# Kernel tuning notes

Measured on AMD Instinct MI355X. Metric: run time of the kernel, lower is better.

## Reference

```python
import jax, jax.numpy as jnp
import numpy as np

B, Hdim, Wdim, C, HEADS, WS = 16, 112, 112, 128, 4, 7
VD = C
MLP_H = int(4.0 * VD)
EPS = 1e-5


def _layernorm(x, g, b):
    mu = jnp.mean(x, axis=-1, keepdims=True)
    var = jnp.mean(jnp.square(x - mu), axis=-1, keepdims=True)
    return (x - mu) * jax.lax.rsqrt(var + EPS) * g + b


def _rel_pos_index(ws):
    # static numpy computation, identical to the torch buffer
    coords = np.stack(np.meshgrid(np.arange(ws), np.arange(ws), indexing='ij'))  # (2, ws, ws)
    cf = coords.reshape(2, -1)                       # (2, N)
    rel = cf[:, :, None] - cf[:, None, :]            # (2, N, N)
    rel = rel.transpose(1, 2, 0).copy()              # (N, N, 2)
    rel[:, :, 0] += ws - 1
    rel[:, :, 1] += ws - 1
    rel[:, :, 0] *= 2 * ws - 1
    return jnp.asarray(rel.sum(-1))                  # (N, N) int


def setup_inputs() -> dict:
    key = jax.random.key(0)
    ks = jax.random.split(key, 10)
    nrm = lambda k, s: jax.random.normal(k, s, jnp.float32) * 0.02
    return {
        'x': jax.random.normal(ks[0], (B, Hdim * Wdim, C), jnp.float32),
        'v': jax.random.normal(ks[1], (B, Hdim * Wdim, C), jnp.float32),
        'norm1_g': jnp.ones((C,), jnp.float32), 'norm1_b': jnp.zeros((C,), jnp.float32),
        'normv_g': jnp.ones((C,), jnp.float32), 'normv_b': jnp.zeros((C,), jnp.float32),
        'q_w': nrm(ks[2], (C, C)), 'q_b': jnp.zeros((C,), jnp.float32),
        'kv_w': nrm(ks[3], (2 * C, C)), 'kv_b': jnp.zeros((2 * C,), jnp.float32),
        'rpb_table': nrm(ks[4], ((2 * WS - 1) ** 2, HEADS)),
        'proj_w': nrm(ks[5], (VD, VD)), 'proj_b': jnp.zeros((VD,), jnp.float32),
        'norm2_g': jnp.ones((VD,), jnp.float32), 'norm2_b': jnp.zeros((VD,), jnp.float32),
        'fc1_w': nrm(ks[6], (MLP_H, VD)), 'fc1_b': jnp.zeros((MLP_H,), jnp.float32),
        'fc2_w': nrm(ks[7], (VD, MLP_H)), 'fc2_b': jnp.zeros((VD,), jnp.float32),
        'H': Hdim, 'W': Wdim,
    }


def reference(x, v, norm1_g, norm1_b, normv_g, normv_b, q_w, q_b, kv_w, kv_b,
              rpb_table, proj_w, proj_b, norm2_g, norm2_b, fc1_w, fc1_b,
              fc2_w, fc2_b, H, W):
    Bsz, L, Cd = x.shape
    ws = WS
    heads = HEADS
    hd = Cd // heads
    scale = hd ** (-0.5)

    xs = _layernorm(x, norm1_g, norm1_b).reshape(Bsz, H, W, Cd)
    vs = _layernorm(v, normv_g, normv_b).reshape(Bsz, H, W, Cd)

    pad_b = (ws - H % ws) % ws
    pad_r = (ws - W % ws) % ws
    if pad_b or pad_r:
        xs = jnp.pad(xs, ((0, 0), (0, pad_b), (0, pad_r), (0, 0)))
        vs = jnp.pad(vs, ((0, 0), (0, pad_b), (0, pad_r), (0, 0)))
    Hp, Wp = H + pad_b, W + pad_r

    def part(t):  # window partition -> (nW*B, ws*ws, C)
        return t.reshape(Bsz, Hp // ws, ws, Wp // ws, ws, t.shape[-1]) \
                .transpose(0, 1, 3, 2, 4, 5).reshape(-1, ws * ws, t.shape[-1])

    xw = part(xs)
    vw = part(vs)
    N = ws * ws

    q = (xw @ q_w.T + q_b).reshape(-1, N, heads, hd).transpose(0, 2, 1, 3)   # (B_, h, N, d)
    kv = (vw @ kv_w.T + kv_b).reshape(-1, N, 2, heads, hd).transpose(2, 0, 3, 1, 4)
    k, vv = kv[0], kv[1]

    attn = jnp.einsum('bhnd,bhmd->bhnm', q * scale, k)
    rpi = _rel_pos_index(ws)
    bias = rpb_table[rpi.reshape(-1)].reshape(N, N, heads).transpose(2, 0, 1)  # (h, N, N)
    attn = jax.nn.softmax(attn + bias[None], axis=-1)

    out = jnp.einsum('bhnm,bhmd->bhnd', attn, vv).transpose(0, 2, 1, 3).reshape(-1, N, Cd)
    out = out @ proj_w.T + proj_b

    # window reverse
    out = out.reshape(Bsz, Hp // ws, Wp // ws, ws, ws, VD) \
             .transpose(0, 1, 3, 2, 4, 5).reshape(Bsz, Hp, Wp, VD)
    out = out[:, :H, :W, :].reshape(Bsz, H * W, VD)

    xo = out + x  # residual with pre-norm shortcut
    h = _layernorm(xo, norm2_g, norm2_b)
    h = jax.nn.gelu(h @ fc1_w.T + fc1_b, approximate=False)
    h = h @ fc2_w.T + fc2_b
    return xo + h
```

## Files before the change

### kernel.cpp

```cpp
#include <hip/hip_runtime.h>
#include <hip/hip_bf16.h>
#include <math.h>

typedef __hip_bfloat16 bf16;
typedef __hip_bfloat162 bf162;
typedef __attribute__((ext_vector_type(8))) short bf16x8;
typedef __attribute__((ext_vector_type(4))) short short4v;
typedef __attribute__((ext_vector_type(4))) float f32x4;

__device__ __forceinline__ float b2f(bf16 x){ return __bfloat162float(x); }
__device__ __forceinline__ bf16  f2b(float x){ return __float2bfloat16(x); }
__device__ __forceinline__ short f2bs(float x){ bf16 h = __float2bfloat16(x); return *(short*)&h; }

constexpr int kH = 112, kW = 112, kC = 128, kHeads = 4, kWS = 7;
constexpr int kN = 49, kHD = 32, kL = kH * kW;
constexpr int kWinElems = kN * kC;
constexpr int kMLP = 512;
constexpr float kEps = 1e-5f;
constexpr float kScale = 0.17677669529663687f;
constexpr int kAP = 136;
constexpr int kHP = 520;
constexpr int kXP = 132;

__global__ __launch_bounds__(256) void k_cvt(
    const float* __restrict__ qw, const float* __restrict__ kvw,
    const float* __restrict__ pw, const float* __restrict__ w1,
    const float* __restrict__ w2, short* __restrict__ dst)
{
    const int i = blockIdx.x * 256 + threadIdx.x;
    float val;
    if (i < 16384)       val = qw[i];
    else if (i < 49152)  val = kvw[i - 16384];
    else if (i < 65536)  val = pw[i - 49152];
    else if (i < 131072) val = w1[i - 65536];
    else                 val = w2[i - 131072];
    dst[i] = f2bs(val);
}

__global__ __launch_bounds__(256) void k_ln_qkv_mfma(
    const float* __restrict__ x, const float* __restrict__ v,
    const float* __restrict__ n1g, const float* __restrict__ n1b,
    const float* __restrict__ nvg, const float* __restrict__ nvb,
    const short* __restrict__ qwb, const float* __restrict__ qb,
    const short* __restrict__ kvwb, const float* __restrict__ kvb,
    bf16* __restrict__ qo, bf16* __restrict__ ko, bf16* __restrict__ vo)
{
    __shared__ short Xs[32 * kAP], Vs[32 * kAP];
    const int tid = threadIdx.x, wave = tid >> 6, lane = tid & 63;
    const int quad = lane >> 4, l16 = lane & 15;
    const int row0 = blockIdx.x * 32;
    const int c0 = lane * 2;

    for (int n = wave; n < 32; n += 4) {
        const size_t r = (size_t)(row0 + n) * kC;
        const float2 xv = *(const float2*)(x + r + c0);
        const float2 vv = *(const float2*)(v + r + c0);
        float sx = xv.x + xv.y, qx = xv.x * xv.x + xv.y * xv.y;
        float sv = vv.x + vv.y, qv = vv.x * vv.x + vv.y * vv.y;
        #pragma unroll
        for (int off = 32; off > 0; off >>= 1) {
            sx += __shfl_xor(sx, off); qx += __shfl_xor(qx, off);
            sv += __shfl_xor(sv, off); qv += __shfl_xor(qv, off);
        }
        const float mux = sx * (1.f / kC);
        const float ivx = rsqrtf(qx * (1.f / kC) - mux * mux + kEps);
        const float muv = sv * (1.f / kC);
        const float ivv = rsqrtf(qv * (1.f / kC) - muv * muv + kEps);
        Xs[n * kAP + c0]     = f2bs((xv.x - mux) * ivx * n1g[c0] + n1b[c0]);
        Xs[n * kAP + c0 + 1] = f2bs((xv.y - mux) * ivx * n1g[c0 + 1] + n1b[c0 + 1]);
        Vs[n * kAP + c0]     = f2bs((vv.x - muv) * ivv * nvg[c0] + nvb[c0]);
        Vs[n * kAP + c0 + 1] = f2bs((vv.y - muv) * ivv * nvg[c0 + 1] + nvb[c0 + 1]);
    }
    __syncthreads();

    int woff[2];
    #pragma unroll
    for (int mt = 0; mt < 2; mt++) {
        const int gr = row0 + mt * 16 + l16;
        const int b = gr / kL, l = gr - b * kL;
        const int h = l / kW, w_ = l - h * kW;
        woff[mt] = ((b << 8) + (h / 7) * 16 + (w_ / 7)) * kWinElems
                 + ((h % 7) * 7 + (w_ % 7)) * kC;
    }

    bf16x8 xf[2][4], vf[2][4];
    #pragma unroll
    for (int mt = 0; mt < 2; mt++)
        #pragma unroll
        for (int ks = 0; ks < 4; ks++) {
            xf[mt][ks] = *(const bf16x8*)&Xs[(mt * 16 + l16) * kAP + ks * 32 + quad * 8];
            vf[mt][ks] = *(const bf16x8*)&Vs[(mt * 16 + l16) * kAP + ks * 32 + quad * 8];
        }

    #pragma unroll
    for (int j = 0; j < 6; j++) {
        const int nt = wave * 6 + j;
        const bool isq = (nt < 8);
        const short* wmat = isq ? qwb : kvwb;
        const int wr0 = (isq ? nt : nt - 8) * 16;
        const float* bias = isq ? qb : kvb;
        const int bidx = wr0 + quad * 4;
        f32x4 a0 = { bias[bidx], bias[bidx + 1], bias[bidx + 2], bias[bidx + 3] };
        f32x4 a1 = a0;
        if (isq) {
            #pragma unroll
            for (int ks = 0; ks < 4; ks++) {
                const bf16x8 af = *(const bf16x8*)(wmat + (size_t)(wr0 + l16) * kC + ks * 32 + quad * 8);
                a0 = __builtin_amdgcn_mfma_f32_16x16x32_bf16(af, xf[0][ks], a0, 0, 0, 0);
                a1 = __builtin_amdgcn_mfma_f32_16x16x32_bf16(af, xf[1][ks], a1, 0, 0, 0);
            }
        } else {
            #pragma unroll
            for (int ks = 0; ks < 4; ks++) {
                const bf16x8 af = *(const bf16x8*)(wmat + (size_t)(wr0 + l16) * kC + ks * 32 + quad * 8);
                a0 = __builtin_amdgcn_mfma_f32_16x16x32_bf16(af, vf[0][ks], a0, 0, 0, 0);
                a1 = __builtin_amdgcn_mfma_f32_16x16x32_bf16(af, vf[1][ks], a1, 0, 0, 0);
            }
        }
        bf16* dst = isq ? qo : (nt < 16 ? ko : vo);
        const int cb = (isq ? nt : (nt < 16 ? nt - 8 : nt - 16)) * 16 + quad * 4;
        short4v p0, p1;
        #pragma unroll
        for (int i = 0; i < 4; i++) { p0[i] = f2bs(a0[i]); p1[i] = f2bs(a1[i]); }
        *(short4v*)((short*)dst + (size_t)woff[0] + cb) = p0;
        *(short4v*)((short*)dst + (size_t)woff[1] + cb) = p1;
    }
}

__global__ __launch_bounds__(256, 3) void k_attn_mfma(
    bf16* __restrict__ qbuf, const bf16* __restrict__ kbuf,
    const bf16* __restrict__ vbuf, const float* __restrict__ rpb)
{
    __shared__ short Pl[kHeads][64 * 64];
    __shared__ short Vt[kHeads][32 * 64];
    __shared__ float rpl[kHeads][169];
    const int tid = threadIdx.x, wave = tid >> 6, lane = tid & 63;
    const int quad = lane >> 4, l16 = lane & 15;
    const int head = wave;
    const size_t wbase = (size_t)blockIdx.x * kWinElems;

    for (int i = lane; i < 169; i += 64) rpl[head][i] = rpb[i * kHeads + head];

    bf16x8 qf[4], kf[4];
    const bf16* qp = qbuf + wbase + head * kHD + quad * 8;
    const bf16* kp = kbuf + wbase + head * kHD + quad * 8;
    #pragma unroll
    for (int t = 0; t < 4; t++) {
        qf[t] = *(const bf16x8*)(qp + (size_t)(t * 16 + l16) * kC);
        kf[t] = *(const bf16x8*)(kp + (size_t)(t * 16 + l16) * kC);
    }

    #pragma unroll
    for (int h = 0; h < 4; h++) {
        for (int i = tid; i < 1024; i += 256) {
            const int m = i >> 4, d2 = (i & 15) << 1;
            int val = 0;
            if (m < 49) val = *(const int*)(vbuf + wbase + (size_t)m * kC + h * kHD + d2);
            Vt[h][d2 * 64 + (m ^ ((d2 & 7) << 3))]         = (short)(val & 0xffff);
            Vt[h][(d2 + 1) * 64 + (m ^ (((d2 + 1) & 7) << 3))] = (short)(val >> 16);
        }
    }

    f32x4 S[4][4];
    #pragma unroll
    for (int nt = 0; nt < 4; nt++)
        #pragma unroll
        for (int mt = 0; mt < 4; mt++)
            S[nt][mt] = __builtin_amdgcn_mfma_f32_16x16x32_bf16(
                qf[nt], kf[mt], (f32x4){0.f, 0.f, 0.f, 0.f}, 0, 0, 0);

    __syncthreads();

    int an[4][4];
    #pragma unroll
    for (int nt = 0; nt < 4; nt++)
        #pragma unroll
        for (int i = 0; i < 4; i++) {
            const int n = nt * 16 + quad * 4 + i;
            an[nt][i] = 13 * (n / 7) + (n % 7) + 84;
        }
    int bm[4]; bool mok[4];
    #pragma unroll
    for (int mt = 0; mt < 4; mt++) {
        const int m = mt * 16 + l16;
        bm[mt] = 13 * (m / 7) + (m % 7);
        mok[mt] = (m < 49);
    }

    const float* rp = rpl[head];
    #pragma unroll
    for (int nt = 0; nt < 4; nt++)
        #pragma unroll
        for (int i = 0; i < 4; i++) {
            float sv[4];
            #pragma unroll
            for (int mt = 0; mt < 4; mt++) {
                int idx = an[nt][i] - bm[mt];
                idx = ((unsigned)idx > 168u) ? 0 : idx;
                sv[mt] = mok[mt] ? (S[nt][mt][i] * kScale + rp[idx]) : -1e30f;
            }
            float mx = fmaxf(fmaxf(sv[0], sv[1]), fmaxf(sv[2], sv[3]));
            #pragma unroll
            for (int off = 1; off < 16; off <<= 1) mx = fmaxf(mx, __shfl_xor(mx, off));
            float e[4];
            float sum = 0.f;
            #pragma unroll
            for (int mt = 0; mt < 4; mt++) { e[mt] = __expf(sv[mt] - mx); sum += e[mt]; }
            #pragma unroll
            for (int off = 1; off < 16; off <<= 1) sum += __shfl_xor(sum, off);
            const float inv = 1.f / sum;
            const int prow = nt * 16 + quad * 4 + i;
            short* pr = &Pl[head][prow * 64];
            const int sw = (prow & 7) << 3;
            #pragma unroll
            for (int mt = 0; mt < 4; mt++)
                pr[(mt * 16 + l16) ^ sw] = f2bs(e[mt] * inv);
        }

    bf16x8 va[2][2], pb2[4][2];
    #pragma unroll
    for (int dt = 0; dt < 2; dt++)
        #pragma unroll
        for (int ks = 0; ks < 2; ks++) {
            const int r = dt * 16 + l16;
            va[dt][ks] = *(const bf16x8*)&Vt[head][r * 64 + ((ks * 32 + quad * 8) ^ ((r & 7) << 3))];
        }
    #pragma unroll
    for (int nt = 0; nt < 4; nt++)
        #pragma unroll
        for (int ks = 0; ks < 2; ks++) {
            const int r = nt * 16 + l16;
            pb2[nt][ks] = *(const bf16x8*)&Pl[head][r * 64 + ((ks * 32 + quad * 8) ^ ((r & 7) << 3))];
        }
    f32x4 o[2][4];
    #pragma unroll
    for (int dt = 0; dt < 2; dt++)
        #pragma unroll
        for (int nt = 0; nt < 4; nt++) {
            f32x4 a = __builtin_amdgcn_mfma_f32_16x16x32_bf16(
                va[dt][0], pb2[nt][0], (f32x4){0.f, 0.f, 0.f, 0.f}, 0, 0, 0);
            o[dt][nt] = __builtin_amdgcn_mfma_f32_16x16x32_bf16(
                va[dt][1], pb2[nt][1], a, 0, 0, 0);
        }

    #pragma unroll
    for (int nt = 0; nt < 4; nt++) {
        const int n = nt * 16 + l16;
        if (n < 49) {
            bf16* dst = qbuf + wbase + (size_t)n * kC + head * kHD + quad * 4;
            #pragma unroll
            for (int dt = 0; dt < 2; dt++) {
                short4v p;
                #pragma unroll
                for (int i = 0; i < 4; i++) p[i] = f2bs(o[dt][nt][i]);
                *(short4v*)(dst + dt * 16) = p;
            }
        }
    }
}

constexpr int kMT = 32;

__global__ __launch_bounds__(256, 3) void k_proj_mlp(
    const bf16* __restrict__ ao, const short* __restrict__ pwb,
    const float* __restrict__ pb, const float* __restrict__ x,
    float* __restrict__ out,
    const float* __restrict__ g2, const float* __restrict__ b2v,
    const short* __restrict__ w1b, const float* __restrict__ bb1,
    const short* __restrict__ w2b, const float* __restrict__ bb2)
{
    __shared__ float Xo[kMT * kXP];
    __shared__ short U[kMT * kHP];
    short* const As  = U;
    short* const A_s = U;
    short* const H_s = U;
    const int tid = threadIdx.x, wave = tid >> 6, lane = tid & 63;
    const int quad = lane >> 4, l16 = lane & 15;
    const size_t row0 = (size_t)blockIdx.x * kMT;
    const int c0 = lane * 2;

    for (int n = wave; n < 32; n += 4) {
        const int gr = (int)row0 + n;
        const int b = gr / kL, l = gr - b * kL;
        const int h = l / kW, w_ = l - h * kW;
        const size_t off = (size_t)(((b << 8) + (h / 7) * 16 + (w_ / 7))) * kWinElems
                         + ((h % 7) * 7 + (w_ % 7)) * kC;
        *(int*)&As[n * kAP + c0] = *(const int*)((const short*)ao + off + c0);
    }
    __syncthreads();

    bf16x8 bfrag[2][4];
    #pragma unroll
    for (int mt = 0; mt < 2; mt++)
        #pragma unroll
        for (int ks = 0; ks < 4; ks++)
            bfrag[mt][ks] = *(const bf16x8*)&As[(mt * 16 + l16) * kAP + ks * 32 + quad * 8];

    float4 res[2][2];
    #pragma unroll
    for (int j = 0; j < 2; j++)
        #pragma unroll
        for (int mt = 0; mt < 2; mt++)
            res[j][mt] = *(const float4*)(x + (row0 + mt * 16 + l16) * kC
                                            + (wave * 2 + j) * 16 + quad * 4);

    #pragma unroll
    for (int j = 0; j < 2; j++) {
        const int nt = wave * 2 + j;
        const int cb = nt * 16 + quad * 4;
        f32x4 a0 = { pb[cb], pb[cb + 1], pb[cb + 2], pb[cb + 3] };
        f32x4 a1 = a0;
        #pragma unroll
        for (int ks = 0; ks < 4; ks++) {
            const bf16x8 af = *(const bf16x8*)(pwb + (size_t)(nt * 16 + l16) * kC + ks * 32 + quad * 8);
            a0 = __builtin_amdgcn_mfma_f32_16x16x32_bf16(af, bfrag[0][ks], a0, 0, 0, 0);
            a1 = __builtin_amdgcn_mfma_f32_16x16x32_bf16(af, bfrag[1][ks], a1, 0, 0, 0);
        }
        #pragma unroll
        for (int mt = 0; mt < 2; mt++) {
            const f32x4 a = mt ? a1 : a0;
            float4 r = res[j][mt];
            r.x += a[0]; r.y += a[1]; r.z += a[2]; r.w += a[3];
            *(float4*)&Xo[(mt * 16 + l16) * kXP + cb] = r;
        }
    }
    __syncthreads();

    const float gg0 = g2[c0], gg1 = g2[c0 + 1];
    const float bv0 = b2v[c0], bv1 = b2v[c0 + 1];
    float2 xv[8];
    #pragma unroll
    for (int it = 0; it < 8; it++)
        xv[it] = *(const float2*)&Xo[(wave + it * 4) * kXP + c0];
    float s[8], q[8];
    #pragma unroll
    for (int it = 0; it < 8; it++) {
        s[it] = xv[it].x + xv[it].y;
        q[it] = xv[it].x * xv[it].x + xv[it].y * xv[it].y;
    }
    #pragma unroll
    for (int off = 32; off > 0; off >>= 1) {
        #pragma unroll
        for (int it = 0; it < 8; it++) {
            s[it] += __shfl_xor(s[it], off);
            q[it] += __shfl_xor(q[it], off);
        }
    }
    #pragma unroll
    for (int it = 0; it < 8; it++) {
        const int n = wave + it * 4;
        const float mu = s[it] * (1.f / kC);
        const float iv = rsqrtf(q[it] * (1.f / kC) - mu * mu + kEps);
        const short h0 = f2bs((xv[it].x - mu) * iv * gg0 + bv0);
        const short h1 = f2bs((xv[it].y - mu) * iv * gg1 + bv1);
        *(int*)&A_s[n * kAP + c0] =
            ((int)(unsigned short)h1 << 16) | (int)(unsigned short)h0;
    }
    __syncthreads();

    bf16x8 bfrag2[2][4];
    #pragma unroll
    for (int mt = 0; mt < 2; mt++)
        #pragma unroll
        for (int ks = 0; ks < 4; ks++)
            bfrag2[mt][ks] = *(const bf16x8*)&A_s[(mt * 16 + l16) * kAP + ks * 32 + quad * 8];
    __syncthreads();

    const short* wbase = w1b + (size_t)(wave * 128 + l16) * kC + quad * 8;
    auto loadw1 = [&](bf16x8* dst, int t) {
        #pragma unroll
        for (int ks = 0; ks < 4; ks++)
            dst[ks] = *(const bf16x8*)(wbase + (size_t)t * (16 * kC) + ks * 32);
    };
    auto mfma8 = [&](f32x4* a, const bf16x8* w) {
        #pragma unroll
        for (int ks = 0; ks < 4; ks++) {
            a[0] = __builtin_amdgcn_mfma_f32_16x16x32_bf16(w[ks], bfrag2[0][ks], a[0], 0, 0, 0);
            a[1] = __builtin_amdgcn_mfma_f32_16x16x32_bf16(w[ks], bfrag2[1][ks], a[1], 0, 0, 0);
        }
    };
    #pragma unroll
    for (int g = 0; g < 2; g++) {
        f32x4 acc[4][2];
        #pragma unroll
        for (int t = 0; t < 4; t++) {
            const float4 bi = *(const float4*)(bb1 + (wave * 8 + g * 4 + t) * 16 + quad * 4);
            acc[t][0] = (f32x4){ bi.x, bi.y, bi.z, bi.w };
            acc[t][1] = acc[t][0];
        }
        bf16x8 wA[4], wB[4];
        loadw1(wA, g * 4 + 0);
        loadw1(wB, g * 4 + 1);
        mfma8(acc[0], wA);
        loadw1(wA, g * 4 + 2);
        mfma8(acc[1], wB);
        loadw1(wB, g * 4 + 3);
        mfma8(acc[2], wA);
        mfma8(acc[3], wB);
        #pragma unroll
        for (int t = 0; t < 4; t++) {
            const int nb = (wave * 8 + g * 4 + t) * 16 + quad * 4;
            #pragma unroll
            for (int mt = 0; mt < 2; mt++) {
                short4v p;
                #pragma unroll
                for (int i = 0; i < 4; i++) {
                    const float a = acc[t][mt][i];
                    p[i] = f2bs(0.5f * a * (1.f + erff(a * 0.70710678118f)));
                }
                *(short4v*)&H_s[(mt * 16 + l16) * kHP + nb] = p;
            }
        }
    }
    __syncthreads();

    const int ct0 = wave * 2;
    f32x4 acc2[2][2];
    #pragma unroll
    for (int t = 0; t < 2; t++) {
        const float4 bi = *(const float4*)(bb2 + (ct0 + t) * 16 + quad * 4);
        acc2[t][0] = (f32x4){ bi.x, bi.y, bi.z, bi.w };
        acc2[t][1] = acc2[t][0];
    }
    const short* w2base = w2b + (size_t)(ct0 * 16 + l16) * kMLP + quad * 8;
    const short* hbase0 = &H_s[l16 * kHP + quad * 8];
    const short* hbase1 = &H_s[(16 + l16) * kHP + quad * 8];
    auto loadh = [&](bf16x8* h, bf16x8* w, int kk) {
        h[0] = *(const bf16x8*)(hbase0 + kk * 32);
        h[1] = *(const bf16x8*)(hbase1 + kk * 32);
        w[0] = *(const bf16x8*)(w2base + kk * 32);
        w[1] = *(const bf16x8*)(w2base + (size_t)16 * kMLP + kk * 32);
    };
    auto mfma4 = [&](const bf16x8* h, const bf16x8* w) {
        acc2[0][0] = __builtin_amdgcn_mfma_f32_16x16x32_bf16(w[0], h[0], acc2[0][0], 0, 0, 0);
        acc2[0][1] = __builtin_amdgcn_mfma_f32_16x16x32_bf16(w[0], h[1], acc2[0][1], 0, 0, 0);
        acc2[1][0] = __builtin_amdgcn_mfma_f32_16x16x32_bf16(w[1], h[0], acc2[1][0], 0, 0, 0);
        acc2[1][1] = __builtin_amdgcn_mfma_f32_16x16x32_bf16(w[1], h[1], acc2[1][1], 0, 0, 0);
    };
    bf16x8 hA[2], wwA[2], hB[2], wwB[2];
    loadh(hA, wwA, 0);
    #pragma unroll
    for (int kk = 0; kk < 16; kk += 2) {
        loadh(hB, wwB, kk + 1);
        mfma4(hA, wwA);
        if (kk + 2 < 16) loadh(hA, wwA, kk + 2);
        mfma4(hB, wwB);
    }

    #pragma unroll
    for (int t = 0; t < 2; t++) {
        const int cbv = (ct0 + t) * 16 + quad * 4;
        #pragma unroll
        for (int mt = 0; mt < 2; mt++) {
            const size_t m = row0 + mt * 16 + l16;
            const float4 xo = *(const float4*)&Xo[(mt * 16 + l16) * kXP + cbv];
            float4 r;
            r.x = xo.x + acc2[t][mt][0]; r.y = xo.y + acc2[t][mt][1];
            r.z = xo.z + acc2[t][mt][2]; r.w = xo.w + acc2[t][mt][3];
            *(float4*)(out + m * kC + cbv) = r;
        }
    }
}

extern "C" void kernel_launch(void* const* d_in, const int* in_sizes, int n_in,
                              void* d_out, int out_size, void* d_ws, size_t ws_size,
                              hipStream_t stream) {
    (void)in_sizes; (void)n_in; (void)out_size; (void)ws_size;
    const float* x      = (const float*)d_in[0];
    const float* v      = (const float*)d_in[1];
    const float* n1g    = (const float*)d_in[2];
    const float* n1b    = (const float*)d_in[3];
    const float* nvg    = (const float*)d_in[4];
    const float* nvb    = (const float*)d_in[5];
    const float* q_w    = (const float*)d_in[6];
    const float* q_b    = (const float*)d_in[7];
    const float* kv_w   = (const float*)d_in[8];
    const float* kv_b   = (const float*)d_in[9];
    const float* rpb    = (const float*)d_in[10];
    const float* proj_w = (const float*)d_in[11];
    const float* proj_b = (const float*)d_in[12];
    const float* n2g    = (const float*)d_in[13];
    const float* n2b    = (const float*)d_in[14];
    const float* fc1_w  = (const float*)d_in[15];
    const float* fc1_b  = (const float*)d_in[16];
    const float* fc2_w  = (const float*)d_in[17];
    const float* fc2_b  = (const float*)d_in[18];

    const size_t winTot = (size_t)4096 * kWinElems;
    bf16* qbuf = (bf16*)d_ws;
    bf16* kbuf = qbuf + winTot;
    bf16* vbuf = kbuf + winTot;
    short* wcvt = (short*)(vbuf + winTot);
    short* qwb  = wcvt;
    short* kvwb = qwb + 16384;
    short* pwb  = kvwb + 32768;
    short* w1b  = pwb + 16384;
    short* w2b  = w1b + 65536;
    float* outb = (float*)d_out;

    k_cvt<<<768, 256, 0, stream>>>(q_w, kv_w, proj_w, fc1_w, fc2_w, wcvt);
    k_ln_qkv_mfma<<<6272, 256, 0, stream>>>(x, v, n1g, n1b, nvg, nvb,
                                            qwb, q_b, kvwb, kv_b, qbuf, kbuf, vbuf);
    k_attn_mfma<<<4096, 256, 0, stream>>>(qbuf, kbuf, vbuf, rpb);
    k_proj_mlp<<<6272, 256, 0, stream>>>(qbuf, pwb, proj_b, x, outb,
                                         n2g, n2b, w1b, fc1_b, w2b, fc2_b);
}
```

Baseline: 726.4 us.

## Keep residual in registers, swizzle LDS, and raise proj/MLP occupancy

Reworks k_proj_mlp so the attention output is loaded directly from global memory into MFMA fragments instead of staged through LDS, and the post-projection residual stays in registers rather than in a float LDS buffer. LayerNorm statistics are reduced with shuffles plus a small LDS scratch area. Padded LDS strides are replaced by an XOR swizzle, which shrinks LDS so launch bounds can ask for 4 blocks per CU. One barrier is removed. The cost is more live registers per thread, which may cause spills at the higher occupancy target, and uncoalesced direct global fragment loads.

New measurement: 733.0 us. Within noise of the previous version (+0.9%).

```diff
diff --git a/kernel.cpp b/kernel.cpp
--- a/kernel.cpp
+++ b/kernel.cpp
@@ -19,8 +19,6 @@
 constexpr float kEps = 1e-5f;
 constexpr float kScale = 0.17677669529663687f;
 constexpr int kAP = 136;
-constexpr int kHP = 520;
-constexpr int kXP = 132;
 
 __global__ __launch_bounds__(256) void k_cvt(
     const float* __restrict__ qw, const float* __restrict__ kvw,
@@ -260,8 +258,10 @@
 }
 
 constexpr int kMT = 32;
-
-__global__ __launch_bounds__(256, 3) void k_proj_mlp(
+constexpr int kAPs = 128;
+constexpr int kHPs = 512;
+
+__global__ __launch_bounds__(256, 4) void k_proj_mlp(
     const bf16* __restrict__ ao, const short* __restrict__ pwb,
     const float* __restrict__ pb, const float* __restrict__ x,
     float* __restrict__ out,
@@ -269,32 +269,32 @@
     const short* __restrict__ w1b, const float* __restrict__ bb1,
     const short* __restrict__ w2b, const float* __restrict__ bb2)
 {
-    __shared__ float Xo[kMT * kXP];
-    __shared__ short U[kMT * kHP];
-    short* const As  = U;
-    short* const A_s = U;
-    short* const H_s = U;
+    __shared__ short LDSu[kMT * kAPs + kMT * kHPs];
+    short* const A_s = LDSu;
+    short* const H_s = LDSu + kMT * kAPs;
+    float* const lnscr = (float*)H_s;
+
     const int tid = threadIdx.x, wave = tid >> 6, lane = tid & 63;
     const int quad = lane >> 4, l16 = lane & 15;
     const size_t row0 = (size_t)blockIdx.x * kMT;
-    const int c0 = lane * 2;
-
-    for (int n = wave; n < 32; n += 4) {
-        const int gr = (int)row0 + n;
+    const int xorm = (l16 & 7) << 3;
+
+    int woff[2];
+    #pragma unroll
+    for (int mt = 0; mt < 2; mt++) {
+        const int gr = (int)row0 + mt * 16 + l16;
         const int b = gr / kL, l = gr - b * kL;
         const int h = l / kW, w_ = l - h * kW;
-        const size_t off = (size_t)(((b << 8) + (h / 7) * 16 + (w_ / 7))) * kWinElems
-                         + ((h % 7) * 7 + (w_ % 7)) * kC;
-        *(int*)&As[n * kAP + c0] = *(const int*)((const short*)ao + off + c0);
-    }
-    __syncthreads();
-
+        woff[mt] = ((b << 8) + (h / 7) * 16 + (w_ / 7)) * kWinElems
+                 + ((h % 7) * 7 + (w_ % 7)) * kC;
+    }
     bf16x8 bfrag[2][4];
     #pragma unroll
     for (int mt = 0; mt < 2; mt++)
         #pragma unroll
         for (int ks = 0; ks < 4; ks++)
-            bfrag[mt][ks] = *(const bf16x8*)&As[(mt * 16 + l16) * kAP + ks * 32 + quad * 8];
+            bfrag[mt][ks] = *(const bf16x8*)((const short*)ao
+                                + (size_t)woff[mt] + ks * 32 + quad * 8);
 
     float4 res[2][2];
     #pragma unroll
@@ -303,12 +303,21 @@
         for (int mt = 0; mt < 2; mt++)
             res[j][mt] = *(const float4*)(x + (row0 + mt * 16 + l16) * kC
                                             + (wave * 2 + j) * 16 + quad * 4);
-
+    float4 gv[2], bvv[2];
+    #pragma unroll
+    for (int j = 0; j < 2; j++) {
+        const int cb = (wave * 2 + j) * 16 + quad * 4;
+        gv[j]  = *(const float4*)(g2 + cb);
+        bvv[j] = *(const float4*)(b2v + cb);
+    }
+
+    f32x4 xo[2][2];
     #pragma unroll
     for (int j = 0; j < 2; j++) {
         const int nt = wave * 2 + j;
         const int cb = nt * 16 + quad * 4;
-        f32x4 a0 = { pb[cb], pb[cb + 1], pb[cb + 2], pb[cb + 3] };
+        const float4 pbv = *(const float4*)(pb + cb);
+        f32x4 a0 = { pbv.x, pbv.y, pbv.z, pbv.w };
         f32x4 a1 = a0;
         #pragma unroll
         for (int ks = 0; ks < 4; ks++) {
@@ -317,44 +326,62 @@
             a1 = __builtin_amdgcn_mfma_f32_16x16x32_bf16(af, bfrag[1][ks], a1, 0, 0, 0);
         }
         #pragma unroll
+        for (int i = 0; i < 4; i++) {
+            xo[j][0][i] = a0[i] + ((const float*)&res[j][0])[i];
+            xo[j][1][i] = a1[i] + ((const float*)&res[j][1])[i];
+        }
+    }
+
+    float sp[2], qp[2];
+    #pragma unroll
+    for (int mt = 0; mt < 2; mt++) {
+        float s = 0.f, q = 0.f;
+        #pragma unroll
+        for (int j = 0; j < 2; j++)
+            #pragma unroll
+            for (int i = 0; i < 4; i++) {
+                const float v = xo[j][mt][i];
+                s += v; q += v * v;
+            }
+        s += __shfl_xor(s, 16); q += __shfl_xor(q, 16);
+        s += __shfl_xor(s, 32); q += __shfl_xor(q, 32);
+        sp[mt] = s; qp[mt] = q;
+    }
+    if (quad == 0) {
+        #pragma unroll
         for (int mt = 0; mt < 2; mt++) {
-            const f32x4 a = mt ? a1 : a0;
-            float4 r = res[j][mt];
-            r.x += a[0]; r.y += a[1]; r.z += a[2]; r.w += a[3];
-            *(float4*)&Xo[(mt * 16 + l16) * kXP + cb] = r;
+            float2 pr; pr.x = sp[mt]; pr.y = qp[mt];
+            *(float2*)&lnscr[(mt * 16 + l16) * 8 + wave * 2] = pr;
         }
     }
     __syncthreads();
 
-    const float gg0 = g2[c0], gg1 = g2[c0 + 1];
-    const float bv0 = b2v[c0], bv1 = b2v[c0 + 1];
-    float2 xv[8];
-    #pragma unroll
-    for (int it = 0; it < 8; it++)
-        xv[it] = *(const float2*)&Xo[(wave + it * 4) * kXP + c0];
-    float s[8], q[8];
-    #pragma unroll
-    for (int it = 0; it < 8; it++) {
-        s[it] = xv[it].x + xv[it].y;
-        q[it] = xv[it].x * xv[it].x + xv[it].y * xv[it].y;
-    }
-    #pragma unroll
-    for (int off = 32; off > 0; off >>= 1) {
-        #pragma unroll
-        for (int it = 0; it < 8; it++) {
-            s[it] += __shfl_xor(s[it], off);
-            q[it] += __shfl_xor(q[it], off);
-        }
-    }
-    #pragma unroll
-    for (int it = 0; it < 8; it++) {
-        const int n = wave + it * 4;
-        const float mu = s[it] * (1.f / kC);
-        const float iv = rsqrtf(q[it] * (1.f / kC) - mu * mu + kEps);
-        const short h0 = f2bs((xv[it].x - mu) * iv * gg0 + bv0);
-        const short h1 = f2bs((xv[it].y - mu) * iv * gg1 + bv1);
-        *(int*)&A_s[n * kAP + c0] =
-            ((int)(unsigned short)h1 << 16) | (int)(unsigned short)h0;
+    float mu[2], iv[2];
+    #pragma unroll
+    for (int mt = 0; mt < 2; mt++) {
+        const int r = mt * 16 + l16;
+        float s = 0.f, q = 0.f;
+        #pragma unroll
+        for (int w = 0; w < 4; w++) {
+            const float2 pr = *(const float2*)&lnscr[r * 8 + w * 2];
+            s += pr.x; q += pr.y;
+        }
+        mu[mt] = s * (1.f / kC);
+        iv[mt] = rsqrtf(q * (1.f / kC) - mu[mt] * mu[mt] + kEps);
+    }
+
+    #pragma unroll
+    for (int j = 0; j < 2; j++) {
+        const int cb = (wave * 2 + j) * 16 + quad * 4;
+        #pragma unroll
+        for (int mt = 0; mt < 2; mt++) {
+            short4v p;
+            #pragma unroll
+            for (int i = 0; i < 4; i++)
+                p[i] = f2bs((xo[j][mt][i] - mu[mt]) * iv[mt]
+                            * ((const float*)&gv[j])[i] + ((const float*)&bvv[j])[i]);
+            *(short4v*)&A_s[(mt * 16 + l16) * kAPs + (cb ^ xorm)] = p;
+        }
     }
     __syncthreads();
 
@@ -363,8 +390,8 @@
     for (int mt = 0; mt < 2; mt++)
         #pragma unroll
         for (int ks = 0; ks < 4; ks++)
-            bfrag2[mt][ks] = *(const bf16x8*)&A_s[(mt * 16 + l16) * kAP + ks * 32 + quad * 8];
-    __syncthreads();
+            bfrag2[mt][ks] = *(const bf16x8*)&A_s[(mt * 16 + l16) * kAPs
+                                + ((ks * 32 + quad * 8) ^ xorm)];
 
     const short* wbase = w1b + (size_t)(wave * 128 + l16) * kC + quad * 8;
     auto loadw1 = [&](bf16x8* dst, int t) {
@@ -408,7 +435,7 @@
                     const float a = acc[t][mt][i];
                     p[i] = f2bs(0.5f * a * (1.f + erff(a * 0.70710678118f)));
                 }
-                *(short4v*)&H_s[(mt * 16 + l16) * kHP + nb] = p;
+                *(short4v*)&H_s[(mt * 16 + l16) * kHPs + (nb ^ xorm)] = p;
             }
         }
     }
@@ -423,11 +450,12 @@
         acc2[t][1] = acc2[t][0];
     }
     const short* w2base = w2b + (size_t)(ct0 * 16 + l16) * kMLP + quad * 8;
-    const short* hbase0 = &H_s[l16 * kHP + quad * 8];
-    const short* hbase1 = &H_s[(16 + l16) * kHP + quad * 8];
+    const short* hb0 = &H_s[l16 * kHPs];
+    const short* hb1 = &H_s[(16 + l16) * kHPs];
     auto loadh = [&](bf16x8* h, bf16x8* w, int kk) {
-        h[0] = *(const bf16x8*)(hbase0 + kk * 32);
-        h[1] = *(const bf16x8*)(hbase1 + kk * 32);
+        const int col = (kk * 32 + quad * 8) ^ xorm;
+        h[0] = *(const bf16x8*)(hb0 + col);
+        h[1] = *(const bf16x8*)(hb1 + col);
         w[0] = *(const bf16x8*)(w2base + kk * 32);
         w[1] = *(const bf16x8*)(w2base + (size_t)16 * kMLP + kk * 32);
     };
@@ -453,10 +481,11 @@
         #pragma unroll
         for (int mt = 0; mt < 2; mt++) {
             const size_t m = row0 + mt * 16 + l16;
-            const float4 xo = *(const float4*)&Xo[(mt * 16 + l16) * kXP + cbv];
             float4 r;
-            r.x = xo.x + acc2[t][mt][0]; r.y = xo.y + acc2[t][mt][1];
-            r.z = xo.z + acc2[t][mt][2]; r.w = xo.w + acc2[t][mt][3];
+            r.x = xo[t][mt][0] + acc2[t][mt][0];
+            r.y = xo[t][mt][1] + acc2[t][mt][1];
+            r.z = xo[t][mt][2] + acc2[t][mt][2];
+            r.w = xo[t][mt][3] + acc2[t][mt][3];
             *(float4*)(out + m * kC + cbv) = r;
         }
     }
```
